# Optimization experiments

Measured on AMD Instinct MI355X. Metric: run time of the kernel, lower is better.

Reference implementation:

```python
import jax, jax.numpy as jnp
import numpy as np

B, N, C = 32, 64, 128   # events, particles/event, channels (hidden==hidden2==out)
NUM_MAPS = 15           # bell_number(2+2)
E = B * N * N
LN_EPS = 1e-5


def setup_inputs() -> dict:
    key = jax.random.key(0)
    ks = jax.random.split(key, 8)
    x = jax.random.normal(ks[0], (E, C), jnp.float32)
    # complete graph with self-loops per event, nodes of event b are b*N..b*N+N-1
    node = np.arange(B * N, dtype=np.int32).reshape(B, N)
    src = np.repeat(node, N, axis=1).reshape(-1)            # i index per edge
    dst = np.tile(node, (1, N)).reshape(-1)                 # j index per edge
    edge_index = jnp.asarray(np.stack([src, dst]), jnp.int32)
    batch = jnp.asarray(np.repeat(np.arange(B, dtype=np.int32), N))
    # params: Linear(C->C), LayerNorm(C), factorized aggregator coeffs
    W_in = jax.random.normal(ks[1], (C, C), jnp.float32) / np.sqrt(C)
    b_in = jnp.zeros((C,), jnp.float32)
    ln_g = jnp.ones((C,), jnp.float32)
    ln_b = jnp.zeros((C,), jnp.float32)
    s0 = np.sqrt(3.0 / NUM_MAPS)
    s1 = np.sqrt(3.0 / C)
    c00 = jax.random.uniform(ks[2], (C, NUM_MAPS), jnp.float32, -s0, s0)
    c01 = jax.random.uniform(ks[3], (C, NUM_MAPS), jnp.float32, -s0, s0)
    c10 = jax.random.uniform(ks[4], (C, C), jnp.float32, -s1, s1)
    c11 = jax.random.uniform(ks[5], (C, C), jnp.float32, -s1, s1)
    return {"x": x, "edge_index": edge_index, "batch": batch,
            "W_in": W_in, "b_in": b_in, "ln_g": ln_g, "ln_b": ln_b,
            "c00": c00, "c01": c01, "c10": c10, "c11": c11}


def reference(x, edge_index, batch, W_in, b_in, ln_g, ln_b, c00, c01, c10, c11):
    # mlp: Linear -> GELU -> LayerNorm (this order, per ModuleList)
    h = x @ W_in.T + b_in
    h = jax.nn.gelu(h, approximate=False)
    mu = h.mean(-1, keepdims=True)
    var = ((h - mu) ** 2).mean(-1, keepdims=True)
    h = (h - mu) / jnp.sqrt(var + LN_EPS) * ln_g + ln_b

    # aggregate_2to2 with reduce='mean': 15 Eq(2->2) permutation-equivariant maps.
    # edge_index/batch describe complete graphs of N nodes per event -> dense view.
    t = h.reshape(B, N, N, C)                 # t[b,i,j,c]
    row = t.mean(axis=2)                      # [B,N,C] mean_j t[b,i,j]
    col = t.mean(axis=1)                      # [B,N,C] mean_i t[b,i,j]
    idx = jnp.arange(N)
    diag = t[:, idx, idx]                     # [B,N,C]
    trace = diag.mean(axis=1)                 # [B,C]
    tot = t.mean(axis=(1, 2))                 # [B,C]
    eye = jnp.eye(N, dtype=t.dtype)[None, :, :, None]

    # factorized coeffs [C_in?, C_out?, 15]; with C_in==C_out the flatten/linear in
    # the torch code makes the FIRST axis the output channel: out = sum map_m @ coeffs[:,:,m].T
    coeffs = c00[:, None, :] * c10[:, :, None] + c01[None, :, :] * c11[:, :, None]

    def proj(a, m):  # a[..., c] -> [..., o] with W[o, c] = coeffs[o, c, m]
        return jnp.einsum('...c,oc->...o', a, coeffs[:, :, m])

    out = proj(t, 0) + proj(t.swapaxes(1, 2), 1)
    out = out + proj(diag, 2)[:, :, None, :] + proj(diag, 3)[:, None, :, :]
    out = out + proj(row, 4)[:, :, None, :] + proj(row, 5)[:, None, :, :]
    out = out + proj(col, 6)[:, :, None, :] + proj(col, 7)[:, None, :, :]
    out = out + proj(trace, 8)[:, None, None, :] + proj(tot, 9)[:, None, None, :]
    out = out + eye * (proj(diag, 10)[:, :, None, :]
                       + proj(row, 11)[:, :, None, :]
                       + proj(col, 12)[:, :, None, :])
    out = out + eye * (proj(trace, 13)[:, None, None, :]
                       + proj(tot, 14)[:, None, None, :])

    return jax.nn.gelu(out.reshape(E, C), approximate=False)
```

## Files before the change

### kernel.cpp

```cpp
#include <hip/hip_runtime.h>
#include <hip/hip_bf16.h>


#define B_ 32
#define N_ 64
#define C_ 128
#define E_ (B_ * N_ * N_)
#define LN_EPS 1e-5f

typedef unsigned int u32;
typedef unsigned short u16;
typedef short bf16x8 __attribute__((ext_vector_type(8)));
typedef float f32x16 __attribute__((ext_vector_type(16)));

union FragU { uint4 u; bf16x8 v; };

__device__ inline float bf_u16(u16 u) { return __uint_as_float(((u32)u) << 16); }
__device__ inline u32 pack_bf2(float a, float b) {
    __hip_bfloat16 ha = __float2bfloat16(a), hb = __float2bfloat16(b);
    u16 ra = *reinterpret_cast<u16*>(&ha), rb = *reinterpret_cast<u16*>(&hb);
    return (u32)ra | ((u32)rb << 16);
}
__device__ inline u16 pack_bf1(float a) {
    __hip_bfloat16 ha = __float2bfloat16(a);
    return *reinterpret_cast<u16*>(&ha);
}
__device__ inline float b2f(__hip_bfloat16 v) { return __bfloat162float(v); }
__device__ inline float geluf(float v) {
    float v2 = v * v;
    float w = fmaf(0.044715f * v2, v, v);
    float e = __builtin_amdgcn_exp2f(2.3022083f * w);
    return v - v * __builtin_amdgcn_rcpf(e + 1.0f);
}
__device__ inline float ld1(const void* p, int i, int isbf) {
    if (isbf) return b2f(((const __hip_bfloat16*)p)[i]);
    return ((const float*)p)[i];
}
__device__ inline int bf_flag(const void* gp) {
    return (((const u32*)gp)[0] == 0x3F803F80u) ? 1 : 0;
}

#define O_T      ((size_t)0)
#define O_ROW    ((size_t)33554432)
#define O_DIAG   ((size_t)35651584)
#define O_CT     ((size_t)36732928)
#define O_WF     ((size_t)37715968)
#define O_CF     ((size_t)37748736)
#define O_U      ((size_t)37912576)
#define O_V      ((size_t)38961152)
#define O_DGN    ((size_t)40026112)

__global__ void pack_all(const void* __restrict__ W,
                         const void* __restrict__ c00, const void* __restrict__ c01,
                         const void* __restrict__ c10, const void* __restrict__ c11,
                         const void* __restrict__ gp,
                         uint4* __restrict__ WF, uint4* __restrict__ CF,
                         float* __restrict__ cT) {
    int isbf = bf_flag(gp);
    if (blockIdx.x < 24) {
        int idx = blockIdx.x * 256 + threadIdx.x;
        if (idx < 2048) {
            int l = idx & 63, s = (idx >> 6) & 7, ot = idx >> 9;
            int n = ot * 32 + (l & 31), k0 = s * 16 + (l >> 5) * 8;
            float v[8];
#pragma unroll
            for (int j = 0; j < 8; ++j) v[j] = ld1(W, n * 128 + k0 + j, isbf);
            uint4 o;
            o.x = pack_bf2(v[0], v[1]); o.y = pack_bf2(v[2], v[3]);
            o.z = pack_bf2(v[4], v[5]); o.w = pack_bf2(v[6], v[7]);
            WF[(s * 4 + ot) * 64 + l] = o;
        } else {
            int id2 = idx - 2048;
            int mat = id2 >> 11, r = id2 & 2047;
            int l = r & 63, s = (r >> 6) & 7, ot = r >> 9;
            int n = ot * 32 + (l & 31), k0 = s * 16 + (l >> 5) * 8;
            float v[8];
#pragma unroll
            for (int j = 0; j < 8; ++j) {
                int k = k0 + j;
                v[j] = ld1(c00, n * 15 + mat, isbf) * ld1(c10, n * 128 + k, isbf) +
                       ld1(c01, k * 15 + mat, isbf) * ld1(c11, n * 128 + k, isbf);
            }
            uint4 o;
            o.x = pack_bf2(v[0], v[1]); o.y = pack_bf2(v[2], v[3]);
            o.z = pack_bf2(v[4], v[5]); o.w = pack_bf2(v[6], v[7]);
            CF[mat * 2048 + (s * 4 + ot) * 64 + l] = o;
        }
    } else {
        int idx2 = (blockIdx.x - 24) * 256 + threadIdx.x;
        int m = idx2 >> 14, rem = idx2 & 16383;
        int c = rem >> 7, o = rem & 127;
        float val = ld1(c00, o * 15 + m, isbf) * ld1(c10, o * 128 + c, isbf) +
                    ld1(c01, c * 15 + m, isbf) * ld1(c11, o * 128 + c, isbf);
        cT[(m * 128 + c) * 128 + o] = val;
    }
}

__global__ void __launch_bounds__(256) gemm_ln_mfma(const void* __restrict__ x,
                                                    const uint4* __restrict__ WF,
                                                    const void* __restrict__ bp, const void* __restrict__ gp,
                                                    const void* __restrict__ lbp,
                                                    u16* __restrict__ t,
                                                    float* __restrict__ row_sum, float* __restrict__ diag) {
    __shared__ __align__(16) u16 tls[128 * 128];
    __shared__ float rsbuf[4][128];
    uint4* wfl = (uint4*)tls;
    int w = threadIdx.x >> 6, l = threadIdx.x & 63;
    int m = l & 31, hh = l >> 5;
    int isbf = bf_flag(gp);
    int e0 = blockIdx.x * 128;
    int arow = e0 + w * 32 + m;

#pragma unroll
    for (int k = 0; k < 8; ++k) {
        int idx = k * 256 + threadIdx.x;
        wfl[idx] = WF[idx];
    }

    FragU af[8];
    if (isbf) {
#pragma unroll
        for (int s = 0; s < 8; ++s)
            af[s].u = *(const uint4*)((const u16*)x + arow * 128 + s * 16 + hh * 8);
    } else {
        const float* xf = (const float*)x;
#pragma unroll
        for (int s = 0; s < 8; ++s) {
            int k0 = s * 16 + hh * 8;
            float4 f0 = *(const float4*)(xf + arow * 128 + k0);
            float4 f1 = *(const float4*)(xf + arow * 128 + k0 + 4);
            af[s].u.x = pack_bf2(f0.x, f0.y); af[s].u.y = pack_bf2(f0.z, f0.w);
            af[s].u.z = pack_bf2(f1.x, f1.y); af[s].u.w = pack_bf2(f1.z, f1.w);
        }
    }
    __syncthreads();

    f32x16 acc[4];
#pragma unroll
    for (int ot = 0; ot < 4; ++ot)
#pragma unroll
        for (int r = 0; r < 16; ++r) acc[ot][r] = 0.f;

#pragma unroll
    for (int s = 0; s < 8; ++s) {
#pragma unroll
        for (int ot = 0; ot < 4; ++ot) {
            FragU bf;
            bf.u = wfl[(s * 4 + ot) * 64 + l];
            acc[ot] = __builtin_amdgcn_mfma_f32_32x32x16_bf16(af[s].v, bf.v, acc[ot], 0, 0, 0);
        }
    }

    float bias[4], gsc[4], bof[4];
#pragma unroll
    for (int ot = 0; ot < 4; ++ot) {
        int o = ot * 32 + m;
        bias[ot] = ld1(bp, o, isbf);
        gsc[ot] = ld1(gp, o, isbf);
        bof[ot] = ld1(lbp, o, isbf);
    }
#pragma unroll
    for (int ot = 0; ot < 4; ++ot)
#pragma unroll
        for (int r = 0; r < 16; ++r) acc[ot][r] = geluf(acc[ot][r] + bias[ot]);

    __syncthreads();

    float rsum[4] = {0.f, 0.f, 0.f, 0.f};
#pragma unroll
    for (int r = 0; r < 16; ++r) {
        float s = acc[0][r] + acc[1][r] + acc[2][r] + acc[3][r];
        float s2 = acc[0][r] * acc[0][r] + acc[1][r] * acc[1][r] +
                   acc[2][r] * acc[2][r] + acc[3][r] * acc[3][r];
#pragma unroll
        for (int off = 1; off < 32; off <<= 1) {
            s += __shfl_xor(s, off);
            s2 += __shfl_xor(s2, off);
        }
        float mean = s * (1.0f / 128.0f);
        float var = s2 * (1.0f / 128.0f) - mean * mean;
        float rstd = rsqrtf(var + LN_EPS);
        int row = (r & 3) + 8 * (r >> 2) + 4 * hh;
#pragma unroll
        for (int ot = 0; ot < 4; ++ot) {
            int o = ot * 32 + m;
            float y = (acc[ot][r] - mean) * rstd * gsc[ot] + bof[ot];
            rsum[ot] += y;
            tls[(w * 32 + row) * 128 + o] = pack_bf1(y);
        }
    }
#pragma unroll
    for (int ot = 0; ot < 4; ++ot) {
        rsum[ot] += __shfl_xor(rsum[ot], 32);
        rsbuf[w][ot * 32 + m] = rsum[ot];
    }
    __syncthreads();

    int b = e0 >> 12, i0 = (e0 >> 6) & 63;
    {
        int p = threadIdx.x >> 7, c = threadIdx.x & 127;
        int ni = b * 64 + i0 + p;
        row_sum[ni * 128 + c] = rsbuf[2 * p][c] + rsbuf[2 * p + 1][c];
        diag[ni * 128 + c] = bf_u16(tls[(p * 64 + i0 + p) * 128 + c]);
    }
#pragma unroll
    for (int q = 0; q < 8; ++q) {
        int chunk = q * 256 + threadIdx.x;
        int row = chunk >> 4, c16 = chunk & 15;
        uint4 v = *(const uint4*)&tls[row * 128 + c16 * 8];
        *(uint4*)&t[(e0 + row) * 128 + c16 * 8] = v;
    }
}

__global__ void __launch_bounds__(512) uvall_kernel(const u16* __restrict__ t,
                                                    const float* __restrict__ row_sum,
                                                    const float* __restrict__ diag,
                                                    const float* __restrict__ cT,
                                                    float* __restrict__ U, float* __restrict__ V,
                                                    float* __restrict__ DgN) {
    __shared__ float dg[4][128], rm[4][128], cm[4][128];
    __shared__ float trs[128], tts[128];
    __shared__ float pU[4][4][128], pV[4][4][128], pD[4][4][128];
    __shared__ float paw[4][128], pad_[4][128];
    int b = blockIdx.x >> 4, n0 = (blockIdx.x & 15) * 4;
    int tid = threadIdx.x;
    int o = tid & 127, cq = tid >> 7;

    {
        int g = (b * 64 + n0 + cq) * 128 + o;
        dg[cq][o] = diag[g];
        rm[cq][o] = row_sum[g] * (1.0f / 64.0f);
    }
    float cs[4];
#pragma unroll
    for (int nn = 0; nn < 4; ++nn) {
        size_t base = (((size_t)(b << 12) + (n0 + nn)) << 7) + o + ((size_t)cq << 17);
        float s = 0.f;
#pragma unroll
        for (int i = 0; i < 16; ++i) s += bf_u16(t[base + ((size_t)i << 13)]);
        cs[nn] = s;
    }
    float tr = 0.f, tt = 0.f;
#pragma unroll
    for (int n = 0; n < 16; ++n) {
        int g = (b * 64 + cq * 16 + n) * 128 + o;
        tr += diag[g];
        tt += row_sum[g];
    }
#pragma unroll
    for (int nn = 0; nn < 4; ++nn) pU[cq][nn][o] = cs[nn];
    paw[cq][o] = tr;
    pad_[cq][o] = tt;
    __syncthreads();
    cm[cq][o] = (pU[0][cq][o] + pU[1][cq][o] + pU[2][cq][o] + pU[3][cq][o]) * (1.0f / 64.0f);
    if (cq == 0) trs[o] = (paw[0][o] + paw[1][o] + paw[2][o] + paw[3][o]) * (1.0f / 64.0f);
    if (cq == 1) tts[o] = (pad_[0][o] + pad_[1][o] + pad_[2][o] + pad_[3][o]) * (1.0f / 4096.0f);
    __syncthreads();

    float aU[4] = {0}, aV[4] = {0}, aD[4] = {0}, aw = 0.f, ad = 0.f;
    int c0 = cq * 32;
    for (int cc = 0; cc < 32; ++cc) {
        int c = c0 + cc;
        float c2 = cT[(2 * 128 + c) * 128 + o], c4 = cT[(4 * 128 + c) * 128 + o], c6 = cT[(6 * 128 + c) * 128 + o];
        float c3 = cT[(3 * 128 + c) * 128 + o], c5 = cT[(5 * 128 + c) * 128 + o], c7 = cT[(7 * 128 + c) * 128 + o];
        float cA = cT[(10 * 128 + c) * 128 + o], cB = cT[(11 * 128 + c) * 128 + o], cC = cT[(12 * 128 + c) * 128 + o];
        float c8 = cT[(8 * 128 + c) * 128 + o], c9 = cT[(9 * 128 + c) * 128 + o];
        float cD = cT[(13 * 128 + c) * 128 + o], cE = cT[(14 * 128 + c) * 128 + o];
        float trv = trs[c], ttv = tts[c];
        aw += c8 * trv + c9 * ttv;
        ad += cD * trv + cE * ttv;
#pragma unroll
        for (int nn = 0; nn < 4; ++nn) {
            float d = dg[nn][c], r = rm[nn][c], cl = cm[nn][c];
            aU[nn] += c2 * d + c4 * r + c6 * cl;
            aV[nn] += c3 * d + c5 * r + c7 * cl;
            aD[nn] += cA * d + cB * r + cC * cl;
        }
    }
#pragma unroll
    for (int nn = 0; nn < 4; ++nn) {
        pU[cq][nn][o] = aU[nn];
        pV[cq][nn][o] = aV[nn];
        pD[cq][nn][o] = aD[nn];
    }
    paw[cq][o] = aw;
    pad_[cq][o] = ad;
    __syncthreads();
    {
        int nn = cq;
        float u = pU[0][nn][o] + pU[1][nn][o] + pU[2][nn][o] + pU[3][nn][o];
        float v = pV[0][nn][o] + pV[1][nn][o] + pV[2][nn][o] + pV[3][nn][o];
        float d = pD[0][nn][o] + pD[1][nn][o] + pD[2][nn][o] + pD[3][nn][o];
        float w = paw[0][o] + paw[1][o] + paw[2][o] + paw[3][o];
        float a = pad_[0][o] + pad_[1][o] + pad_[2][o] + pad_[3][o];
        int g = (b * 64 + n0 + nn) * 128 + o;
        U[g] = u + w;
        V[g] = v;
        DgN[g] = d + a;
    }
}

__global__ void __launch_bounds__(256) final_mfma(const u16* __restrict__ t,
                                                  const uint4* __restrict__ CF,
                                                  const float* __restrict__ U, const float* __restrict__ V,
                                                  const float* __restrict__ DgN, const void* __restrict__ gp,
                                                  void* __restrict__ outp) {
    __shared__ __align__(16) uint4 cfl[2048];
    u16* ols = (u16*)cfl;
    int w = threadIdx.x >> 6, l = threadIdx.x & 63;
    int m = l & 31, hh = l >> 5;
    int e0 = blockIdx.x * 128;
    int b = e0 >> 12;
    int i0 = (e0 >> 6) & 63;
    int iw = i0 + (w >> 1);
    int jA = (w & 1) * 32 + m;
    const u16* ai_base = t + (size_t)(e0 + w * 32 + m) * 128;
    const u16* aj_base = t + (size_t)((b << 12) + (jA << 6) + iw) * 128;

#pragma unroll
    for (int k = 0; k < 8; ++k) {
        int idx = k * 256 + threadIdx.x;
        cfl[idx] = CF[idx];
    }

    FragU af[8], ag[8];
#pragma unroll
    for (int s = 0; s < 8; ++s) {
        int k0 = s * 16 + hh * 8;
        af[s].u = *(const uint4*)(ai_base + k0);
        ag[s].u = *(const uint4*)(aj_base + k0);
    }
    __syncthreads();

    f32x16 acc[4];
#pragma unroll
    for (int ot = 0; ot < 4; ++ot)
#pragma unroll
        for (int r = 0; r < 16; ++r) acc[ot][r] = 0.f;

#pragma unroll
    for (int s = 0; s < 8; ++s) {
#pragma unroll
        for (int ot = 0; ot < 4; ++ot) {
            FragU b0;
            b0.u = cfl[(s * 4 + ot) * 64 + l];
            acc[ot] = __builtin_amdgcn_mfma_f32_32x32x16_bf16(af[s].v, b0.v, acc[ot], 0, 0, 0);
        }
    }
    __syncthreads();
#pragma unroll
    for (int k = 0; k < 8; ++k) {
        int idx = k * 256 + threadIdx.x;
        cfl[idx] = CF[2048 + idx];
    }
    __syncthreads();
#pragma unroll
    for (int s = 0; s < 8; ++s) {
#pragma unroll
        for (int ot = 0; ot < 4; ++ot) {
            FragU b1;
            b1.u = cfl[(s * 4 + ot) * 64 + l];
            acc[ot] = __builtin_amdgcn_mfma_f32_32x32x16_bf16(ag[s].v, b1.v, acc[ot], 0, 0, 0);
        }
    }

    int ni = b * 64 + iw;
    int isbf = bf_flag(gp);
    float uw[4], dg4[4];
#pragma unroll
    for (int ot = 0; ot < 4; ++ot) {
        int o = ot * 32 + m;
        uw[ot] = U[ni * 128 + o];
        dg4[ot] = DgN[ni * 128 + o];
    }
    if (isbf) {
        __syncthreads();
#pragma unroll
        for (int r = 0; r < 16; ++r) {
            int row = (r & 3) + 8 * (r >> 2) + 4 * hh;
            int jD = (w & 1) * 32 + row;
            int nj = b * 64 + jD;
            bool dia = (jD == iw);
#pragma unroll
            for (int ot = 0; ot < 4; ++ot) {
                int o = ot * 32 + m;
                float val = acc[ot][r] + uw[ot] + V[nj * 128 + o];
                if (dia) val += dg4[ot];
                ols[(w * 32 + row) * 128 + o] = pack_bf1(geluf(val));
            }
        }
        __syncthreads();
        u16* ob = (u16*)outp;
#pragma unroll
        for (int q = 0; q < 8; ++q) {
            int chunk = q * 256 + threadIdx.x;
            int row = chunk >> 4, c16 = chunk & 15;
            uint4 v = *(const uint4*)&ols[row * 128 + c16 * 8];
            *(uint4*)&ob[(e0 + row) * 128 + c16 * 8] = v;
        }
    } else {
        float* ob = (float*)outp;
#pragma unroll
        for (int r = 0; r < 16; ++r) {
            int row = (r & 3) + 8 * (r >> 2) + 4 * hh;
            int jD = (w & 1) * 32 + row;
            int e = e0 + w * 32 + row;
            int nj = b * 64 + jD;
            bool dia = (jD == iw);
#pragma unroll
            for (int ot = 0; ot < 4; ++ot) {
                int o = ot * 32 + m;
                float val = acc[ot][r] + uw[ot] + V[nj * 128 + o];
                if (dia) val += dg4[ot];
                ob[e * 128 + o] = geluf(val);
            }
        }
    }
}

extern "C" void kernel_launch(void* const* d_in, const int* in_sizes, int n_in,
                              void* d_out, int out_size, void* d_ws, size_t ws_size,
                              hipStream_t stream) {
    const void* x = d_in[0];
    const void* W = d_in[3];
    const void* bp = d_in[4];
    const void* gp = d_in[5];
    const void* lbp = d_in[6];
    const void* c00 = d_in[7];
    const void* c01 = d_in[8];
    const void* c10 = d_in[9];
    const void* c11 = d_in[10];

    char* ws = (char*)d_ws;
    u16* t16 = (u16*)(ws + O_T);
    float* row_sum = (float*)(ws + O_ROW);
    float* diag = (float*)(ws + O_DIAG);
    float* cT = (float*)(ws + O_CT);
    uint4* WF = (uint4*)(ws + O_WF);
    uint4* CF = (uint4*)(ws + O_CF);
    float* Uarr = (float*)(ws + O_U);
    float* Varr = (float*)(ws + O_V);
    float* DgN = (float*)(ws + O_DGN);

    pack_all<<<984, 256, 0, stream>>>(W, c00, c01, c10, c11, gp, WF, CF, cT);
    gemm_ln_mfma<<<E_ / 128, 256, 0, stream>>>(x, WF, bp, gp, lbp, t16, row_sum, diag);
    uvall_kernel<<<B_ * 16, 512, 0, stream>>>(t16, row_sum, diag, cT, Uarr, Varr, DgN);
    final_mfma<<<E_ / 128, 256, 0, stream>>>(t16, CF, Uarr, Varr, DgN, gp, (void*)d_out);
}
```

Before: 199.8 us.

## Split output channels across waves and keep weight fragments in registers

Result: slower. 248.4 us (+24.3%).

```diff
diff --git a/kernel.cpp b/kernel.cpp
--- a/kernel.cpp
+++ b/kernel.cpp
@@ -96,119 +96,105 @@
     }
 }
 
-__global__ void __launch_bounds__(256) gemm_ln_mfma(const void* __restrict__ x,
-                                                    const uint4* __restrict__ WF,
-                                                    const void* __restrict__ bp, const void* __restrict__ gp,
-                                                    const void* __restrict__ lbp,
-                                                    u16* __restrict__ t,
-                                                    float* __restrict__ row_sum, float* __restrict__ diag) {
-    __shared__ __align__(16) u16 tls[128 * 128];
-    __shared__ float rsbuf[4][128];
-    uint4* wfl = (uint4*)tls;
+__global__ void __launch_bounds__(256, 4) gemm_ln_mfma(const void* __restrict__ x,
+                                                       const uint4* __restrict__ WF,
+                                                       const void* __restrict__ bp, const void* __restrict__ gp,
+                                                       const void* __restrict__ lbp,
+                                                       u16* __restrict__ t,
+                                                       float* __restrict__ row_sum, float* __restrict__ diag) {
+    __shared__ __align__(16) u16 tls[64 * 128];
+    __shared__ float sp[4][64][2];
     int w = threadIdx.x >> 6, l = threadIdx.x & 63;
     int m = l & 31, hh = l >> 5;
     int isbf = bf_flag(gp);
-    int e0 = blockIdx.x * 128;
-    int arow = e0 + w * 32 + m;
-
-#pragma unroll
-    for (int k = 0; k < 8; ++k) {
-        int idx = k * 256 + threadIdx.x;
-        wfl[idx] = WF[idx];
-    }
-
-    FragU af[8];
-    if (isbf) {
+    int e0 = blockIdx.x * 64;
+    int b = e0 >> 12, i = (e0 >> 6) & 63;
+    int o = w * 32 + m;
+    float bias_l = ld1(bp, o, isbf), g_l = ld1(gp, o, isbf), bo_l = ld1(lbp, o, isbf);
+
+    FragU bfr[8];
+#pragma unroll
+    for (int s = 0; s < 8; ++s) bfr[s].u = WF[(s * 4 + w) * 64 + l];
+
+    f32x16 acc[2];
+#pragma unroll
+    for (int g = 0; g < 2; ++g)
+#pragma unroll
+        for (int r = 0; r < 16; ++r) acc[g][r] = 0.f;
+
+#pragma unroll
+    for (int g = 0; g < 2; ++g) {
+        int arow = e0 + g * 32 + m;
+        FragU af[8];
+        if (isbf) {
+#pragma unroll
+            for (int s = 0; s < 8; ++s)
+                af[s].u = *(const uint4*)((const u16*)x + (size_t)arow * 128 + s * 16 + hh * 8);
+        } else {
+            const float* xf = (const float*)x;
+#pragma unroll
+            for (int s = 0; s < 8; ++s) {
+                int k0 = s * 16 + hh * 8;
+                float4 f0 = *(const float4*)(xf + (size_t)arow * 128 + k0);
+                float4 f1 = *(const float4*)(xf + (size_t)arow * 128 + k0 + 4);
+                af[s].u.x = pack_bf2(f0.x, f0.y); af[s].u.y = pack_bf2(f0.z, f0.w);
+                af[s].u.z = pack_bf2(f1.x, f1.y); af[s].u.w = pack_bf2(f1.z, f1.w);
+            }
+        }
 #pragma unroll
         for (int s = 0; s < 8; ++s)
-            af[s].u = *(const uint4*)((const u16*)x + arow * 128 + s * 16 + hh * 8);
-    } else {
-        const float* xf = (const float*)x;
-#pragma unroll
-        for (int s = 0; s < 8; ++s) {
-            int k0 = s * 16 + hh * 8;
-            float4 f0 = *(const float4*)(xf + arow * 128 + k0);
-            float4 f1 = *(const float4*)(xf + arow * 128 + k0 + 4);
-            af[s].u.x = pack_bf2(f0.x, f0.y); af[s].u.y = pack_bf2(f0.z, f0.w);
-            af[s].u.z = pack_bf2(f1.x, f1.y); af[s].u.w = pack_bf2(f1.z, f1.w);
-        }
-    }
-    __syncthreads();
-
-    f32x16 acc[4];
-#pragma unroll
-    for (int ot = 0; ot < 4; ++ot)
-#pragma unroll
-        for (int r = 0; r < 16; ++r) acc[ot][r] = 0.f;
-
-#pragma unroll
-    for (int s = 0; s < 8; ++s) {
-#pragma unroll
-        for (int ot = 0; ot < 4; ++ot) {
-            FragU bf;
-            bf.u = wfl[(s * 4 + ot) * 64 + l];
-            acc[ot] = __builtin_amdgcn_mfma_f32_32x32x16_bf16(af[s].v, bf.v, acc[ot], 0, 0, 0);
-        }
-    }
-
-    float bias[4], gsc[4], bof[4];
-#pragma unroll
-    for (int ot = 0; ot < 4; ++ot) {
-        int o = ot * 32 + m;
-        bias[ot] = ld1(bp, o, isbf);
-        gsc[ot] = ld1(gp, o, isbf);
-        bof[ot] = ld1(lbp, o, isbf);
-    }
-#pragma unroll
-    for (int ot = 0; ot < 4; ++ot)
-#pragma unroll
-        for (int r = 0; r < 16; ++r) acc[ot][r] = geluf(acc[ot][r] + bias[ot]);
-
-    __syncthreads();
-
-    float rsum[4] = {0.f, 0.f, 0.f, 0.f};
-#pragma unroll
-    for (int r = 0; r < 16; ++r) {
-        float s = acc[0][r] + acc[1][r] + acc[2][r] + acc[3][r];
-        float s2 = acc[0][r] * acc[0][r] + acc[1][r] * acc[1][r] +
-                   acc[2][r] * acc[2][r] + acc[3][r] * acc[3][r];
-#pragma unroll
-        for (int off = 1; off < 32; off <<= 1) {
-            s += __shfl_xor(s, off);
-            s2 += __shfl_xor(s2, off);
-        }
-        float mean = s * (1.0f / 128.0f);
-        float var = s2 * (1.0f / 128.0f) - mean * mean;
-        float rstd = rsqrtf(var + LN_EPS);
-        int row = (r & 3) + 8 * (r >> 2) + 4 * hh;
-#pragma unroll
-        for (int ot = 0; ot < 4; ++ot) {
-            int o = ot * 32 + m;
-            float y = (acc[ot][r] - mean) * rstd * gsc[ot] + bof[ot];
-            rsum[ot] += y;
-            tls[(w * 32 + row) * 128 + o] = pack_bf1(y);
-        }
-    }
-#pragma unroll
-    for (int ot = 0; ot < 4; ++ot) {
-        rsum[ot] += __shfl_xor(rsum[ot], 32);
-        rsbuf[w][ot * 32 + m] = rsum[ot];
-    }
-    __syncthreads();
-
-    int b = e0 >> 12, i0 = (e0 >> 6) & 63;
-    {
-        int p = threadIdx.x >> 7, c = threadIdx.x & 127;
-        int ni = b * 64 + i0 + p;
-        row_sum[ni * 128 + c] = rsbuf[2 * p][c] + rsbuf[2 * p + 1][c];
-        diag[ni * 128 + c] = bf_u16(tls[(p * 64 + i0 + p) * 128 + c]);
-    }
-#pragma unroll
-    for (int q = 0; q < 8; ++q) {
+            acc[g] = __builtin_amdgcn_mfma_f32_32x32x16_bf16(af[s].v, bfr[s].v, acc[g], 0, 0, 0);
+    }
+
+#pragma unroll
+    for (int g = 0; g < 2; ++g)
+#pragma unroll
+        for (int r = 0; r < 16; ++r) acc[g][r] = geluf(acc[g][r] + bias_l);
+
+#pragma unroll
+    for (int g = 0; g < 2; ++g)
+#pragma unroll
+        for (int r = 0; r < 16; ++r) {
+            float v = acc[g][r];
+            float s = v, s2 = v * v;
+#pragma unroll
+            for (int off = 1; off < 32; off <<= 1) {
+                s += __shfl_xor(s, off);
+                s2 += __shfl_xor(s2, off);
+            }
+            if (m == 0) {
+                int j = g * 32 + (r & 3) + 8 * (r >> 2) + 4 * hh;
+                sp[w][j][0] = s;
+                sp[w][j][1] = s2;
+            }
+        }
+    __syncthreads();
+
+    float rsum = 0.f;
+    int ni = b * 64 + i;
+#pragma unroll
+    for (int g = 0; g < 2; ++g)
+#pragma unroll
+        for (int r = 0; r < 16; ++r) {
+            int j = g * 32 + (r & 3) + 8 * (r >> 2) + 4 * hh;
+            float S = sp[0][j][0] + sp[1][j][0] + sp[2][j][0] + sp[3][j][0];
+            float S2 = sp[0][j][1] + sp[1][j][1] + sp[2][j][1] + sp[3][j][1];
+            float mean = S * (1.0f / 128.0f);
+            float var = S2 * (1.0f / 128.0f) - mean * mean;
+            float rstd = rsqrtf(var + LN_EPS);
+            float y = (acc[g][r] - mean) * rstd * g_l + bo_l;
+            rsum += y;
+            tls[j * 128 + o] = pack_bf1(y);
+            if (j == i) diag[(size_t)ni * 128 + o] = y;
+        }
+    rsum += __shfl_xor(rsum, 32);
+    if (l < 32) row_sum[(size_t)ni * 128 + o] = rsum;
+
+    __syncthreads();
+#pragma unroll
+    for (int q = 0; q < 4; ++q) {
         int chunk = q * 256 + threadIdx.x;
-        int row = chunk >> 4, c16 = chunk & 15;
-        uint4 v = *(const uint4*)&tls[row * 128 + c16 * 8];
-        *(uint4*)&t[(e0 + row) * 128 + c16 * 8] = v;
+        *(uint4*)&t[(size_t)e0 * 128 + chunk * 8] = *(const uint4*)&tls[chunk * 8];
     }
 }
 
@@ -300,119 +286,79 @@
     }
 }
 
-__global__ void __launch_bounds__(256) final_mfma(const u16* __restrict__ t,
-                                                  const uint4* __restrict__ CF,
-                                                  const float* __restrict__ U, const float* __restrict__ V,
-                                                  const float* __restrict__ DgN, const void* __restrict__ gp,
-                                                  void* __restrict__ outp) {
-    __shared__ __align__(16) uint4 cfl[2048];
-    u16* ols = (u16*)cfl;
+__global__ void __launch_bounds__(256, 4) final_mfma(const u16* __restrict__ t,
+                                                     const uint4* __restrict__ CF,
+                                                     const float* __restrict__ U, const float* __restrict__ V,
+                                                     const float* __restrict__ DgN, const void* __restrict__ gp,
+                                                     void* __restrict__ outp) {
     int w = threadIdx.x >> 6, l = threadIdx.x & 63;
     int m = l & 31, hh = l >> 5;
     int e0 = blockIdx.x * 128;
-    int b = e0 >> 12;
-    int i0 = (e0 >> 6) & 63;
-    int iw = i0 + (w >> 1);
-    int jA = (w & 1) * 32 + m;
-    const u16* ai_base = t + (size_t)(e0 + w * 32 + m) * 128;
-    const u16* aj_base = t + (size_t)((b << 12) + (jA << 6) + iw) * 128;
-
-#pragma unroll
-    for (int k = 0; k < 8; ++k) {
-        int idx = k * 256 + threadIdx.x;
-        cfl[idx] = CF[idx];
-    }
-
-    FragU af[8], ag[8];
+    int b = e0 >> 12, i0 = (e0 >> 6) & 63;
+    int o = w * 32 + m;
+    int isbf = bf_flag(gp);
+
+    FragU b0[8], b1[8];
 #pragma unroll
     for (int s = 0; s < 8; ++s) {
-        int k0 = s * 16 + hh * 8;
-        af[s].u = *(const uint4*)(ai_base + k0);
-        ag[s].u = *(const uint4*)(aj_base + k0);
-    }
-    __syncthreads();
-
-    f32x16 acc[4];
-#pragma unroll
-    for (int ot = 0; ot < 4; ++ot)
-#pragma unroll
-        for (int r = 0; r < 16; ++r) acc[ot][r] = 0.f;
-
-#pragma unroll
-    for (int s = 0; s < 8; ++s) {
-#pragma unroll
-        for (int ot = 0; ot < 4; ++ot) {
-            FragU b0;
-            b0.u = cfl[(s * 4 + ot) * 64 + l];
-            acc[ot] = __builtin_amdgcn_mfma_f32_32x32x16_bf16(af[s].v, b0.v, acc[ot], 0, 0, 0);
-        }
-    }
-    __syncthreads();
-#pragma unroll
-    for (int k = 0; k < 8; ++k) {
-        int idx = k * 256 + threadIdx.x;
-        cfl[idx] = CF[2048 + idx];
-    }
-    __syncthreads();
-#pragma unroll
-    for (int s = 0; s < 8; ++s) {
-#pragma unroll
-        for (int ot = 0; ot < 4; ++ot) {
-            FragU b1;
-            b1.u = cfl[(s * 4 + ot) * 64 + l];
-            acc[ot] = __builtin_amdgcn_mfma_f32_32x32x16_bf16(ag[s].v, b1.v, acc[ot], 0, 0, 0);
-        }
-    }
-
-    int ni = b * 64 + iw;
-    int isbf = bf_flag(gp);
-    float uw[4], dg4[4];
-#pragma unroll
-    for (int ot = 0; ot < 4; ++ot) {
-        int o = ot * 32 + m;
-        uw[ot] = U[ni * 128 + o];
-        dg4[ot] = DgN[ni * 128 + o];
-    }
-    if (isbf) {
-        __syncthreads();
-#pragma unroll
-        for (int r = 0; r < 16; ++r) {
-            int row = (r & 3) + 8 * (r >> 2) + 4 * hh;
-            int jD = (w & 1) * 32 + row;
-            int nj = b * 64 + jD;
-            bool dia = (jD == iw);
-#pragma unroll
-            for (int ot = 0; ot < 4; ++ot) {
-                int o = ot * 32 + m;
-                float val = acc[ot][r] + uw[ot] + V[nj * 128 + o];
-                if (dia) val += dg4[ot];
-                ols[(w * 32 + row) * 128 + o] = pack_bf1(geluf(val));
-            }
-        }
-        __syncthreads();
-        u16* ob = (u16*)outp;
-#pragma unroll
-        for (int q = 0; q < 8; ++q) {
-            int chunk = q * 256 + threadIdx.x;
-            int row = chunk >> 4, c16 = chunk & 15;
-            uint4 v = *(const uint4*)&ols[row * 128 + c16 * 8];
-            *(uint4*)&ob[(e0 + row) * 128 + c16 * 8] = v;
-        }
-    } else {
-        float* ob = (float*)outp;
-#pragma unroll
-        for (int r = 0; r < 16; ++r) {
-            int row = (r & 3) + 8 * (r >> 2) + 4 * hh;
-            int jD = (w & 1) * 32 + row;
-            int e = e0 + w * 32 + row;
-            int nj = b * 64 + jD;
-            bool dia = (jD == iw);
-#pragma unroll
-            for (int ot = 0; ot < 4; ++ot) {
-                int o = ot * 32 + m;
-                float val = acc[ot][r] + uw[ot] + V[nj * 128 + o];
-                if (dia) val += dg4[ot];
-                ob[e * 128 + o] = geluf(val);
+        b0[s].u = CF[(s * 4 + w) * 64 + l];
+        b1[s].u = CF[2048 + (s * 4 + w) * 64 + l];
+    }
+
+#pragma unroll
+    for (int g = 0; g < 4; ++g) {
+        int iw = i0 + (g >> 1);
+        int ja = (g & 1) * 32 + m;
+        const u16* ai = t + (size_t)(e0 + g * 32 + m) * 128;
+        const u16* aj = t + (size_t)((b << 12) + (ja << 6) + iw) * 128;
+
+        f32x16 acc;
+#pragma unroll
+        for (int r = 0; r < 16; ++r) acc[r] = 0.f;
+
+#pragma unroll
+        for (int c4 = 0; c4 < 2; ++c4) {
+            FragU af[4];
+#pragma unroll
+            for (int s = 0; s < 4; ++s)
+                af[s].u = *(const uint4*)(ai + (c4 * 4 + s) * 16 + hh * 8);
+#pragma unroll
+            for (int s = 0; s < 4; ++s)
+                acc = __builtin_amdgcn_mfma_f32_32x32x16_bf16(af[s].v, b0[c4 * 4 + s].v, acc, 0, 0, 0);
+        }
+#pragma unroll
+        for (int c4 = 0; c4 < 2; ++c4) {
+            FragU ag[4];
+#pragma unroll
+            for (int s = 0; s < 4; ++s)
+                ag[s].u = *(const uint4*)(aj + (c4 * 4 + s) * 16 + hh * 8);
+#pragma unroll
+            for (int s = 0; s < 4; ++s)
+                acc = __builtin_amdgcn_mfma_f32_32x32x16_bf16(ag[s].v, b1[c4 * 4 + s].v, acc, 0, 0, 0);
+        }
+
+        int ni = b * 64 + iw;
+        float uw = U[(size_t)ni * 128 + o];
+        float dgv = DgN[(size_t)ni * 128 + o];
+        if (isbf) {
+            u16* ob = (u16*)outp;
+#pragma unroll
+            for (int r = 0; r < 16; ++r) {
+                int rl = (r & 3) + 8 * (r >> 2) + 4 * hh;
+                int jD = (g & 1) * 32 + rl;
+                float val = acc[r] + uw + V[(size_t)(b * 64 + jD) * 128 + o];
+                if (jD == iw) val += dgv;
+                ob[(size_t)(e0 + g * 32 + rl) * 128 + o] = pack_bf1(geluf(val));
+            }
+        } else {
+            float* ob = (float*)outp;
+#pragma unroll
+            for (int r = 0; r < 16; ++r) {
+                int rl = (r & 3) + 8 * (r >> 2) + 4 * hh;
+                int jD = (g & 1) * 32 + rl;
+                float val = acc[r] + uw + V[(size_t)(b * 64 + jD) * 128 + o];
+                if (jD == iw) val += dgv;
+                ob[(size_t)(e0 + g * 32 + rl) * 128 + o] = geluf(val);
             }
         }
     }
@@ -443,7 +389,7 @@
     float* DgN = (float*)(ws + O_DGN);
 
     pack_all<<<984, 256, 0, stream>>>(W, c00, c01, c10, c11, gp, WF, CF, cT);
-    gemm_ln_mfma<<<E_ / 128, 256, 0, stream>>>(x, WF, bp, gp, lbp, t16, row_sum, diag);
+    gemm_ln_mfma<<<E_ / 64, 256, 0, stream>>>(x, WF, bp, gp, lbp, t16, row_sum, diag);
     uvall_kernel<<<B_ * 16, 512, 0, stream>>>(t16, row_sum, diag, cT, Uarr, Varr, DgN);
     final_mfma<<<E_ / 128, 256, 0, stream>>>(t16, CF, Uarr, Varr, DgN, gp, (void*)d_out);
 }
```

## Retile Linear+GELU+LayerNorm kernel to 64-row blocks with 2x2 wave split

Applied to the files above, without the earlier changes.

Measured after the change: 204.8 us. 1.02x slower.

```diff
diff --git a/kernel.cpp b/kernel.cpp
--- a/kernel.cpp
+++ b/kernel.cpp
@@ -96,119 +96,125 @@
     }
 }
 
-__global__ void __launch_bounds__(256) gemm_ln_mfma(const void* __restrict__ x,
-                                                    const uint4* __restrict__ WF,
-                                                    const void* __restrict__ bp, const void* __restrict__ gp,
-                                                    const void* __restrict__ lbp,
-                                                    u16* __restrict__ t,
-                                                    float* __restrict__ row_sum, float* __restrict__ diag) {
-    __shared__ __align__(16) u16 tls[128 * 128];
-    __shared__ float rsbuf[4][128];
-    uint4* wfl = (uint4*)tls;
-    int w = threadIdx.x >> 6, l = threadIdx.x & 63;
+__global__ void __launch_bounds__(256, 4) gemm_ln_mfma(const void* __restrict__ x,
+                                                       const uint4* __restrict__ WF,
+                                                       const void* __restrict__ bp, const void* __restrict__ gp,
+                                                       const void* __restrict__ lbp,
+                                                       u16* __restrict__ t,
+                                                       float* __restrict__ row_sum, float* __restrict__ diag) {
+    __shared__ __align__(16) u16 atile[64 * 128];
+    __shared__ float sp[2][64][2];
+    __shared__ float rsbuf[2][128];
+    int tid = threadIdx.x;
+    int w = tid >> 6, l = tid & 63;
+    int wr = w >> 1, wc = w & 1;
     int m = l & 31, hh = l >> 5;
     int isbf = bf_flag(gp);
-    int e0 = blockIdx.x * 128;
-    int arow = e0 + w * 32 + m;
-
-#pragma unroll
-    for (int k = 0; k < 8; ++k) {
-        int idx = k * 256 + threadIdx.x;
-        wfl[idx] = WF[idx];
-    }
-
-    FragU af[8];
-    if (isbf) {
-#pragma unroll
-        for (int s = 0; s < 8; ++s)
-            af[s].u = *(const uint4*)((const u16*)x + arow * 128 + s * 16 + hh * 8);
-    } else {
-        const float* xf = (const float*)x;
-#pragma unroll
-        for (int s = 0; s < 8; ++s) {
-            int k0 = s * 16 + hh * 8;
-            float4 f0 = *(const float4*)(xf + arow * 128 + k0);
-            float4 f1 = *(const float4*)(xf + arow * 128 + k0 + 4);
-            af[s].u.x = pack_bf2(f0.x, f0.y); af[s].u.y = pack_bf2(f0.z, f0.w);
-            af[s].u.z = pack_bf2(f1.x, f1.y); af[s].u.w = pack_bf2(f1.z, f1.w);
-        }
-    }
-    __syncthreads();
-
-    f32x16 acc[4];
-#pragma unroll
-    for (int ot = 0; ot < 4; ++ot)
+    int e0 = blockIdx.x * 64;
+    int b = e0 >> 12, i = (e0 >> 6) & 63;
+
+    FragU bfr[16];
+#pragma unroll
+    for (int s = 0; s < 8; ++s)
+#pragma unroll
+        for (int ot = 0; ot < 2; ++ot)
+            bfr[s * 2 + ot].u = WF[(s * 4 + wc * 2 + ot) * 64 + l];
+
+#pragma unroll
+    for (int q = 0; q < 4; ++q) {
+        int c = q * 256 + tid;
+        int row = c >> 4, c16 = c & 15;
+        int sw = (c16 * 16) ^ ((row & 15) << 4);
+        uint4 val;
+        if (isbf) {
+            val = *(const uint4*)((const u16*)x + (size_t)(e0 + row) * 128 + c16 * 8);
+        } else {
+            const float* xf = (const float*)x + (size_t)(e0 + row) * 128 + c16 * 8;
+            float4 f0 = *(const float4*)xf;
+            float4 f1 = *(const float4*)(xf + 4);
+            val.x = pack_bf2(f0.x, f0.y); val.y = pack_bf2(f0.z, f0.w);
+            val.z = pack_bf2(f1.x, f1.y); val.w = pack_bf2(f1.z, f1.w);
+        }
+        *(uint4*)((char*)atile + row * 256 + sw) = val;
+    }
+    __syncthreads();
+
+    f32x16 acc[2];
+#pragma unroll
+    for (int ot = 0; ot < 2; ++ot)
 #pragma unroll
         for (int r = 0; r < 16; ++r) acc[ot][r] = 0.f;
 
+    int arow = wr * 32 + m;
+    const char* abase = (const char*)atile + arow * 256;
+    int amask = (arow & 15) << 4;
 #pragma unroll
     for (int s = 0; s < 8; ++s) {
-#pragma unroll
-        for (int ot = 0; ot < 4; ++ot) {
-            FragU bf;
-            bf.u = wfl[(s * 4 + ot) * 64 + l];
-            acc[ot] = __builtin_amdgcn_mfma_f32_32x32x16_bf16(af[s].v, bf.v, acc[ot], 0, 0, 0);
-        }
-    }
-
-    float bias[4], gsc[4], bof[4];
-#pragma unroll
-    for (int ot = 0; ot < 4; ++ot) {
-        int o = ot * 32 + m;
-        bias[ot] = ld1(bp, o, isbf);
-        gsc[ot] = ld1(gp, o, isbf);
-        bof[ot] = ld1(lbp, o, isbf);
-    }
-#pragma unroll
-    for (int ot = 0; ot < 4; ++ot)
-#pragma unroll
-        for (int r = 0; r < 16; ++r) acc[ot][r] = geluf(acc[ot][r] + bias[ot]);
-
-    __syncthreads();
-
-    float rsum[4] = {0.f, 0.f, 0.f, 0.f};
+        FragU af;
+        af.u = *(const uint4*)(abase + ((s * 32 + hh * 16) ^ amask));
+        acc[0] = __builtin_amdgcn_mfma_f32_32x32x16_bf16(af.v, bfr[s * 2 + 0].v, acc[0], 0, 0, 0);
+        acc[1] = __builtin_amdgcn_mfma_f32_32x32x16_bf16(af.v, bfr[s * 2 + 1].v, acc[1], 0, 0, 0);
+    }
+
+    int o0 = wc * 64 + m, o1 = o0 + 32;
+    float bias0 = ld1(bp, o0, isbf), bias1 = ld1(bp, o1, isbf);
+    float g0 = ld1(gp, o0, isbf), g1 = ld1(gp, o1, isbf);
+    float bo0 = ld1(lbp, o0, isbf), bo1 = ld1(lbp, o1, isbf);
+
 #pragma unroll
     for (int r = 0; r < 16; ++r) {
-        float s = acc[0][r] + acc[1][r] + acc[2][r] + acc[3][r];
-        float s2 = acc[0][r] * acc[0][r] + acc[1][r] * acc[1][r] +
-                   acc[2][r] * acc[2][r] + acc[3][r] * acc[3][r];
+        acc[0][r] = geluf(acc[0][r] + bias0);
+        acc[1][r] = geluf(acc[1][r] + bias1);
+    }
+
+#pragma unroll
+    for (int r = 0; r < 16; ++r) {
+        float s = acc[0][r] + acc[1][r];
+        float s2 = acc[0][r] * acc[0][r] + acc[1][r] * acc[1][r];
 #pragma unroll
         for (int off = 1; off < 32; off <<= 1) {
             s += __shfl_xor(s, off);
             s2 += __shfl_xor(s2, off);
         }
-        float mean = s * (1.0f / 128.0f);
-        float var = s2 * (1.0f / 128.0f) - mean * mean;
+        if (m == 0) {
+            int j = wr * 32 + (r & 3) + 8 * (r >> 2) + 4 * hh;
+            sp[wc][j][0] = s;
+            sp[wc][j][1] = s2;
+        }
+    }
+    __syncthreads();
+
+    u16* tls = atile;
+    float rsum0 = 0.f, rsum1 = 0.f;
+    int ni = b * 64 + i;
+#pragma unroll
+    for (int r = 0; r < 16; ++r) {
+        int j = wr * 32 + (r & 3) + 8 * (r >> 2) + 4 * hh;
+        float S = sp[0][j][0] + sp[1][j][0];
+        float S2 = sp[0][j][1] + sp[1][j][1];
+        float mean = S * (1.0f / 128.0f);
+        float var = S2 * (1.0f / 128.0f) - mean * mean;
         float rstd = rsqrtf(var + LN_EPS);
-        int row = (r & 3) + 8 * (r >> 2) + 4 * hh;
-#pragma unroll
-        for (int ot = 0; ot < 4; ++ot) {
-            int o = ot * 32 + m;
-            float y = (acc[ot][r] - mean) * rstd * gsc[ot] + bof[ot];
-            rsum[ot] += y;
-            tls[(w * 32 + row) * 128 + o] = pack_bf1(y);
-        }
-    }
-#pragma unroll
-    for (int ot = 0; ot < 4; ++ot) {
-        rsum[ot] += __shfl_xor(rsum[ot], 32);
-        rsbuf[w][ot * 32 + m] = rsum[ot];
-    }
-    __syncthreads();
-
-    int b = e0 >> 12, i0 = (e0 >> 6) & 63;
-    {
-        int p = threadIdx.x >> 7, c = threadIdx.x & 127;
-        int ni = b * 64 + i0 + p;
-        row_sum[ni * 128 + c] = rsbuf[2 * p][c] + rsbuf[2 * p + 1][c];
-        diag[ni * 128 + c] = bf_u16(tls[(p * 64 + i0 + p) * 128 + c]);
-    }
-#pragma unroll
-    for (int q = 0; q < 8; ++q) {
-        int chunk = q * 256 + threadIdx.x;
-        int row = chunk >> 4, c16 = chunk & 15;
-        uint4 v = *(const uint4*)&tls[row * 128 + c16 * 8];
-        *(uint4*)&t[(e0 + row) * 128 + c16 * 8] = v;
+        float y0 = (acc[0][r] - mean) * rstd * g0 + bo0;
+        float y1 = (acc[1][r] - mean) * rstd * g1 + bo1;
+        rsum0 += y0; rsum1 += y1;
+        tls[j * 128 + o0] = pack_bf1(y0);
+        tls[j * 128 + o1] = pack_bf1(y1);
+        if (j == i) {
+            diag[(size_t)ni * 128 + o0] = y0;
+            diag[(size_t)ni * 128 + o1] = y1;
+        }
+    }
+    rsum0 += __shfl_xor(rsum0, 32);
+    rsum1 += __shfl_xor(rsum1, 32);
+    if (l < 32) { rsbuf[wr][o0] = rsum0; rsbuf[wr][o1] = rsum1; }
+    __syncthreads();
+
+    if (tid < 128) row_sum[(size_t)ni * 128 + tid] = rsbuf[0][tid] + rsbuf[1][tid];
+#pragma unroll
+    for (int q = 0; q < 4; ++q) {
+        int c = q * 256 + tid;
+        *(uint4*)&t[(size_t)e0 * 128 + c * 8] = *(const uint4*)&tls[c * 8];
     }
 }
 
@@ -443,7 +449,7 @@
     float* DgN = (float*)(ws + O_DGN);
 
     pack_all<<<984, 256, 0, stream>>>(W, c00, c01, c10, c11, gp, WF, CF, cT);
-    gemm_ln_mfma<<<E_ / 128, 256, 0, stream>>>(x, WF, bp, gp, lbp, t16, row_sum, diag);
+    gemm_ln_mfma<<<E_ / 64, 256, 0, stream>>>(x, WF, bp, gp, lbp, t16, row_sum, diag);
     uvall_kernel<<<B_ * 16, 512, 0, stream>>>(t16, row_sum, diag, cT, Uarr, Varr, DgN);
     final_mfma<<<E_ / 128, 256, 0, stream>>>(t16, CF, Uarr, Varr, DgN, gp, (void*)d_out);
 }
```
